# Kernel tuning notes

Measured on AMD Instinct MI355X. Metric: run time of the kernel, lower is better.

Reference implementation:

```python
import jax, jax.numpy as jnp
import numpy as np

EPS = 1e-5

def setup_inputs() -> dict:
    key = jax.random.key(0)
    kx, kw, kb = jax.random.split(key, 3)
    batch, input_dim, embed_dim = 32768, 64, 128
    x = jax.random.normal(kx, (batch, input_dim), dtype=jnp.float32)
    # Per-feature Linear(1, embed_dim): weight row W[i] and bias b[i].
    # torch Linear(1, D) init: U(-1, 1) since fan_in = 1.
    W = jax.random.uniform(kw, (input_dim, embed_dim), dtype=jnp.float32, minval=-1.0, maxval=1.0)
    b = jax.random.uniform(kb, (input_dim, embed_dim), dtype=jnp.float32, minval=-1.0, maxval=1.0)
    gamma = jnp.ones((embed_dim,), dtype=jnp.float32)
    beta = jnp.zeros((embed_dim,), dtype=jnp.float32)
    return {"x": x, "W": W, "b": b, "gamma": gamma, "beta": beta}

def reference(x, W, b, gamma, beta):
    # Fused form of the per-feature Linear(1,D) loop:
    # out[b,i,d] = x[b,i] * W[i,d] + b[i,d]
    e = x[:, :, None] * W[None, :, :] + b[None, :, :]  # [B, F, D]
    mean = jnp.mean(e, axis=-1, keepdims=True)
    var = jnp.mean(jnp.square(e - mean), axis=-1, keepdims=True)
    normed = (e - mean) * jax.lax.rsqrt(var + EPS)
    return normed * gamma + beta
```

## Files before the change

### kernel.cpp

```cpp
#include <hip/hip_runtime.h>

#define LN_EPS 1e-5f


__global__ __launch_bounds__(256) void tabemb_ln_kernel(
    const float* __restrict__ x,
    const float* __restrict__ W,
    const float* __restrict__ b,
    const float* __restrict__ gamma,
    const float* __restrict__ beta,
    float* __restrict__ out,
    int batch)
{
    const int gw   = (blockIdx.x << 2) + (threadIdx.x >> 6);
    const int lane = threadIdx.x & 63;
    const int half = lane >> 5;
    const int l    = lane & 31;
    const int fp   = gw & 31;
    const int i    = (fp << 1) + half;
    const int d0   = l << 2;

    const float4 w4  = *(const float4*)(W     + (i << 7) + d0);
    const float4 b4  = *(const float4*)(b     + (i << 7) + d0);
    const float4 g4  = *(const float4*)(gamma + d0);
    const float4 be4 = *(const float4*)(beta  + d0);

    const int    bstart  = gw >> 5;
    const int    bstride = 256;
    const size_t rowoff  = ((size_t)i << 7) + (size_t)d0;

    for (int bt = bstart; bt < batch; bt += bstride) {
        const float xv = x[(bt << 6) + i];

        float4 e;
        e.x = fmaf(xv, w4.x, b4.x);
        e.y = fmaf(xv, w4.y, b4.y);
        e.z = fmaf(xv, w4.z, b4.z);
        e.w = fmaf(xv, w4.w, b4.w);

        float s  = e.x + e.y + e.z + e.w;
        float s2 = fmaf(e.x, e.x, fmaf(e.y, e.y, fmaf(e.z, e.z, e.w * e.w)));

        #pragma unroll
        for (int m = 1; m <= 16; m <<= 1) {
            s  += __shfl_xor(s,  m, 64);
            s2 += __shfl_xor(s2, m, 64);
        }

        const float mean = s * 0.0078125f;
        const float var  = fmaf(-mean, mean, s2 * 0.0078125f);
        const float inv  = rsqrtf(var + LN_EPS);

        float4 o; float c1, c0;
        c1 = inv * g4.x; c0 = fmaf(-mean, c1, be4.x); o.x = fmaf(e.x, c1, c0);
        c1 = inv * g4.y; c0 = fmaf(-mean, c1, be4.y); o.y = fmaf(e.y, c1, c0);
        c1 = inv * g4.z; c0 = fmaf(-mean, c1, be4.z); o.z = fmaf(e.z, c1, c0);
        c1 = inv * g4.w; c0 = fmaf(-mean, c1, be4.w); o.w = fmaf(e.w, c1, c0);

        *(float4*)(out + (size_t)bt * 8192 + rowoff) = o;
    }
}

extern "C" void kernel_launch(void* const* d_in, const int* in_sizes, int n_in,
                              void* d_out, int out_size, void* d_ws, size_t ws_size,
                              hipStream_t stream) {
    const float* x     = (const float*)d_in[0];
    const float* W     = (const float*)d_in[1];
    const float* b     = (const float*)d_in[2];
    const float* gamma = (const float*)d_in[3];
    const float* beta  = (const float*)d_in[4];
    float* out = (float*)d_out;

    const int batch = in_sizes[0] / 64;

    tabemb_ln_kernel<<<2048, 256, 0, stream>>>(x, W, b, gamma, beta, out, batch);
}
```

Baseline: 1.114 ms.

## Precompute per-feature LayerNorm moments analytically and prefetch next x value

Because each embedding row is affine in the scalar x, the mean and variance over the embed dimension are written as a linear and a quadratic polynomial in x. Their coefficients come from W and b and are reduced once per thread before the batch loop. This removes the per-row cross-lane shuffle reductions, leaving a few FMAs and one rsqrt per row. It also software-prefetches the next x value. The kernel writes a large output, so it is likely store-bandwidth bound and the saving in ALU and shuffle work may be small; the closed-form variance can differ slightly numerically.

After: 1.087 ms. 1.02x faster.

```diff
diff --git a/kernel.cpp b/kernel.cpp
--- a/kernel.cpp
+++ b/kernel.cpp
@@ -25,39 +25,53 @@
     const float4 g4  = *(const float4*)(gamma + d0);
     const float4 be4 = *(const float4*)(beta  + d0);
 
+    float sw = (w4.x + w4.y) + (w4.z + w4.w);
+    float sb = (b4.x + b4.y) + (b4.z + b4.w);
+    #pragma unroll
+    for (int m = 1; m <= 16; m <<= 1) {
+        sw += __shfl_xor(sw, m, 64);
+        sb += __shfl_xor(sb, m, 64);
+    }
+    const float mW = sw * 0.0078125f;
+    const float mB = sb * 0.0078125f;
+
+    const float dw0 = w4.x - mW, dw1 = w4.y - mW, dw2 = w4.z - mW, dw3 = w4.w - mW;
+    const float db0 = b4.x - mB, db1 = b4.y - mB, db2 = b4.z - mB, db3 = b4.w - mB;
+    float sww = fmaf(dw0, dw0, fmaf(dw1, dw1, fmaf(dw2, dw2, dw3 * dw3)));
+    float swb = fmaf(dw0, db0, fmaf(dw1, db1, fmaf(dw2, db2, dw3 * db3)));
+    float sbb = fmaf(db0, db0, fmaf(db1, db1, fmaf(db2, db2, db3 * db3)));
+    #pragma unroll
+    for (int m = 1; m <= 16; m <<= 1) {
+        sww += __shfl_xor(sww, m, 64);
+        swb += __shfl_xor(swb, m, 64);
+        sbb += __shfl_xor(sbb, m, 64);
+    }
+    const float vW   = sww * 0.0078125f;
+    const float cWB2 = swb * 0.015625f;
+    const float vB   = sbb * 0.0078125f;
+
     const int    bstart  = gw >> 5;
     const int    bstride = 256;
     const size_t rowoff  = ((size_t)i << 7) + (size_t)d0;
 
+    float xv = x[(bstart << 6) + i];
     for (int bt = bstart; bt < batch; bt += bstride) {
-        const float xv = x[(bt << 6) + i];
+        const int btn = bt + bstride;
+        float xn = 0.0f;
+        if (btn < batch) xn = x[(btn << 6) + i];
 
-        float4 e;
-        e.x = fmaf(xv, w4.x, b4.x);
-        e.y = fmaf(xv, w4.y, b4.y);
-        e.z = fmaf(xv, w4.z, b4.z);
-        e.w = fmaf(xv, w4.w, b4.w);
-
-        float s  = e.x + e.y + e.z + e.w;
-        float s2 = fmaf(e.x, e.x, fmaf(e.y, e.y, fmaf(e.z, e.z, e.w * e.w)));
-
-        #pragma unroll
-        for (int m = 1; m <= 16; m <<= 1) {
-            s  += __shfl_xor(s,  m, 64);
-            s2 += __shfl_xor(s2, m, 64);
-        }
-
-        const float mean = s * 0.0078125f;
-        const float var  = fmaf(-mean, mean, s2 * 0.0078125f);
+        const float mean = fmaf(xv, mW, mB);
+        const float var  = fmaf(xv, fmaf(xv, vW, cWB2), vB);
         const float inv  = rsqrtf(var + LN_EPS);
 
-        float4 o; float c1, c0;
-        c1 = inv * g4.x; c0 = fmaf(-mean, c1, be4.x); o.x = fmaf(e.x, c1, c0);
-        c1 = inv * g4.y; c0 = fmaf(-mean, c1, be4.y); o.y = fmaf(e.y, c1, c0);
-        c1 = inv * g4.z; c0 = fmaf(-mean, c1, be4.z); o.z = fmaf(e.z, c1, c0);
-        c1 = inv * g4.w; c0 = fmaf(-mean, c1, be4.w); o.w = fmaf(e.w, c1, c0);
+        float4 o; float e, c1, c0;
+        e = fmaf(xv, w4.x, b4.x); c1 = inv * g4.x; c0 = fmaf(-mean, c1, be4.x); o.x = fmaf(e, c1, c0);
+        e = fmaf(xv, w4.y, b4.y); c1 = inv * g4.y; c0 = fmaf(-mean, c1, be4.y); o.y = fmaf(e, c1, c0);
+        e = fmaf(xv, w4.z, b4.z); c1 = inv * g4.z; c0 = fmaf(-mean, c1, be4.z); o.z = fmaf(e, c1, c0);
+        e = fmaf(xv, w4.w, b4.w); c1 = inv * g4.w; c0 = fmaf(-mean, c1, be4.w); o.w = fmaf(e, c1, c0);
 
         *(float4*)(out + (size_t)bt * 8192 + rowoff) = o;
+        xv = xn;
     }
 }
 
```
